# Optimization experiments

Hardware: AMD Instinct MI355X
Metric: run time of the kernel (lower is better)

The kernel has to match this reference:

```python
import jax, jax.numpy as jnp
import numpy as np

B, C, H, W = 2, 128, 64, 64
NUM_HEADS = 8
GN_GROUPS = 8
GN_EPS = 1e-5


def setup_inputs() -> dict:
    key = jax.random.key(0)
    ks = jax.random.split(key, 11)
    s = 0.02
    return {
        "x": jax.random.normal(ks[0], (B, C, H, W), dtype=jnp.float32),
        "Wq": jax.random.normal(ks[1], (C, C), dtype=jnp.float32) * s,
        "bq": jnp.zeros((C,), dtype=jnp.float32),
        "Wk": jax.random.normal(ks[2], (C, C), dtype=jnp.float32) * s,
        "bk": jnp.zeros((C,), dtype=jnp.float32),
        "Wv": jax.random.normal(ks[3], (C, C), dtype=jnp.float32) * s,
        "bv": jnp.zeros((C,), dtype=jnp.float32),
        "Wo": jax.random.normal(ks[4], (C, C), dtype=jnp.float32) * s,
        "bo": jnp.zeros((C,), dtype=jnp.float32),
        "gn_w": jnp.ones((C,), dtype=jnp.float32),
        "gn_b": jnp.zeros((C,), dtype=jnp.float32),
    }


def reference(x, Wq, bq, Wk, bk, Wv, bv, Wo, bo, gn_w, gn_b):
    b, c, h, w = x.shape
    nh = NUM_HEADS
    dh = c // nh
    scale = dh ** (-0.5)

    # [b, c, h, w] -> [b, N, c]
    x_seq = x.reshape(b, c, h * w).transpose(0, 2, 1)

    def proj(W, bias):
        y = jnp.einsum('bnc,dc->bnd', x_seq, W) + bias  # nn.Linear: x @ W.T + b
        return y.reshape(b, -1, nh, dh).transpose(0, 2, 1, 3)  # [b, nh, N, dh]

    q = proj(Wq, bq)
    k = proj(Wk, bk)
    v = proj(Wv, bv)

    attn = jnp.einsum('bhnd,bhmd->bhnm', q, k) * scale  # [b, nh, N, N]
    attn = jax.nn.softmax(attn, axis=-1)
    out = jnp.einsum('bhnm,bhmd->bhnd', attn, v)        # [b, nh, N, dh]

    out = out.transpose(0, 2, 1, 3).reshape(b, -1, c)   # [b, N, c]
    out = jnp.einsum('bnc,dc->bnd', out, Wo) + bo
    out = out.transpose(0, 2, 1).reshape(b, c, h, w)

    # GroupNorm(8, c) with affine params, then residual
    g = GN_GROUPS
    og = out.reshape(b, g, c // g, h, w)
    mean = jnp.mean(og, axis=(2, 3, 4), keepdims=True)
    var = jnp.var(og, axis=(2, 3, 4), keepdims=True)
    og = (og - mean) * jax.lax.rsqrt(var + GN_EPS)
    normed = og.reshape(b, c, h, w) * gn_w[None, :, None, None] + gn_b[None, :, None, None]
    return normed + x
```

## Files before the change

kernel.cpp:

```cpp
#include <hip/hip_runtime.h>

#define TID ((int)threadIdx.x)

constexpr int Bb  = 2;
constexpr int Cc  = 128;
constexpr int Nn  = 4096;
constexpr int NHh = 8;
constexpr int DHd = 16;
constexpr int NSP = 4;
constexpr float GN_EPS_F = 1e-5f;
constexpr float QSCALE = 0.25f * 1.4426950408889634f;

typedef float  f32x4  __attribute__((ext_vector_type(4)));
typedef float  f32x16 __attribute__((ext_vector_type(16)));
typedef short  s16x8  __attribute__((ext_vector_type(8)));
typedef unsigned short u16x8 __attribute__((ext_vector_type(8)));

#if __has_builtin(__builtin_amdgcn_exp2f)
#define EXP2(x) __builtin_amdgcn_exp2f(x)
#else
#define EXP2(x) exp2f(x)
#endif

constexpr size_t WS_PART = 0;
constexpr size_t WS_LP   = 8192;
constexpr size_t WS_AOP  = WS_LP + (size_t)NSP*16*Nn;
constexpr size_t WS_QBF  = WS_AOP + ((size_t)NSP*Bb*Nn*Cc)/2;
constexpr size_t BF_ELEMS = (size_t)Bb*NHh*Nn*DHd;

__device__ __forceinline__ ushort f2bf(float f) {
    uint u = __builtin_bit_cast(uint, f);
    u += 0x7fffu + ((u >> 16) & 1u);
    return (ushort)(u >> 16);
}
__device__ __forceinline__ float bf2f(ushort u) {
    return __builtin_bit_cast(float, ((uint)u) << 16);
}
__device__ __forceinline__ uint cvt_pk_bf16(float lo, float hi) {
    uint d;
    asm("v_cvt_pk_bf16_f32 %0, %1, %2" : "=v"(d) : "v"(lo), "v"(hi));
    return d;
}

__global__ __launch_bounds__(512) void qkv_kernel(
    const float* __restrict__ x,
    const float* __restrict__ Wq, const float* __restrict__ bq,
    const float* __restrict__ Wk, const float* __restrict__ bk,
    const float* __restrict__ Wv, const float* __restrict__ bv,
    ushort* __restrict__ qbf, ushort* __restrict__ kbf, ushort* __restrict__ vtbf)
{
    const int b  = blockIdx.x >> 7;
    const int n0 = (blockIdx.x & 127) << 5;
    __shared__ float sbuf[4356];
    const float* xb = x + (size_t)b * Cc * Nn;
    for (int i = TID; i < 32 * 128; i += 512) {
        int c = i >> 5, nl = i & 31;
        sbuf[nl * 132 + c] = xb[(size_t)c * Nn + n0 + nl];
    }
    __syncthreads();
    const int d = TID & 127, q4 = TID >> 7;
    float aq[8], ak[8], av[8];
#pragma unroll
    for (int j = 0; j < 8; ++j) { aq[j] = 0.f; ak[j] = 0.f; av[j] = 0.f; }
    const float4* wqp = (const float4*)(Wq + (size_t)d * 128);
    const float4* wkp = (const float4*)(Wk + (size_t)d * 128);
    const float4* wvp = (const float4*)(Wv + (size_t)d * 128);
#pragma unroll 4
    for (int c4 = 0; c4 < 32; ++c4) {
        float4 wq4 = wqp[c4], wk4 = wkp[c4], wv4 = wvp[c4];
#pragma unroll
        for (int j = 0; j < 8; ++j) {
            float4 xv = *(const float4*)&sbuf[(q4*8 + j) * 132 + c4 * 4];
            aq[j] += xv.x*wq4.x + xv.y*wq4.y + xv.z*wq4.z + xv.w*wq4.w;
            ak[j] += xv.x*wk4.x + xv.y*wk4.y + xv.z*wk4.z + xv.w*wk4.w;
            av[j] += xv.x*wv4.x + xv.y*wv4.y + xv.z*wv4.z + xv.w*wv4.w;
        }
    }
    const float bq_ = bq[d], bk_ = bk[d], bv_ = bv[d];

    __syncthreads();
#pragma unroll
    for (int j = 0; j < 8; ++j) sbuf[d * 33 + q4*8 + j] = (aq[j] + bq_) * QSCALE;
    __syncthreads();
    {
        int n = TID & 31, oct = TID >> 5;
        int h = oct >> 1, half8 = oct & 1;
        u16x8 u;
#pragma unroll
        for (int e = 0; e < 8; ++e) u[e] = f2bf(sbuf[(oct*8 + e) * 33 + n]);
        *(u16x8*)(qbf + ((size_t)((b*NHh + h)*Nn + n0 + n)) * DHd + half8*8) = u;
    }
    __syncthreads();
#pragma unroll
    for (int j = 0; j < 8; ++j) sbuf[d * 33 + q4*8 + j] = ak[j] + bk_;
    __syncthreads();
    {
        int n = TID & 31, oct = TID >> 5;
        int h = oct >> 1, half8 = oct & 1;
        u16x8 u;
#pragma unroll
        for (int e = 0; e < 8; ++e) u[e] = f2bf(sbuf[(oct*8 + e) * 33 + n]);
        *(u16x8*)(kbf + ((size_t)((b*NHh + h)*Nn + n0 + n)) * DHd + half8*8) = u;
    }
    __syncthreads();
#pragma unroll
    for (int j = 0; j < 8; ++j) sbuf[d * 33 + q4*8 + j] = av[j] + bv_;
    __syncthreads();
    {
        int dch = TID >> 2, qq = TID & 3;
        u16x8 u;
#pragma unroll
        for (int e = 0; e < 8; ++e) u[e] = f2bf(sbuf[dch * 33 + qq*8 + e]);
        int h = dch >> 4, dd = dch & 15;
        *(u16x8*)(vtbf + ((size_t)(b*NHh + h)*DHd + dd) * Nn + n0 + qq*8) = u;
    }
}

__global__ __launch_bounds__(256, 5) void attn_kernel(
    const ushort* __restrict__ qbf, const ushort* __restrict__ kbf,
    const ushort* __restrict__ vtbf, ushort* __restrict__ aop, float* __restrict__ lp)
{
    const int qt = blockIdx.x & 31;
    const int sp = (blockIdx.x >> 5) & 3;
    const int bh = blockIdx.x >> 7;
    const int q0 = qt << 7;
    const int kvbase = sp << 10;
    const ushort* qb  = qbf  + (size_t)bh * Nn * DHd;
    const ushort* kb  = kbf  + (size_t)bh * Nn * DHd;
    const ushort* vtb = vtbf + (size_t)bh * DHd * Nn;

    __shared__ __align__(16) ushort k_lds[64][16];
    __shared__ __align__(16) ushort vt_lds[16][88];
    __shared__ __align__(16) ushort ps[4][32][88];

    const int wave = TID >> 6, lane = TID & 63;
    const int l31 = lane & 31, hi = lane >> 5;
    const int l15 = lane & 15, g  = lane >> 4;
    const int wq = q0 + wave * 32;

    const s16x8 qfrag = *(const s16x8*)(qb + (size_t)(wq + l31) * DHd + 8 * hi);

    float l_run = 0.0f;
    f32x4 o0 = (f32x4)(0.f), o1 = (f32x4)(0.f);
    ushort* psw = &ps[wave][0][0];

    for (int kv0 = kvbase; kv0 < kvbase + 1024; kv0 += 64) {
        if (TID < 128) {
            *(u16x8*)((char*)&k_lds[0][0] + TID * 16) =
                *(const u16x8*)(kb + (size_t)kv0 * DHd + TID * 8);
        } else {
            int t = TID - 128, r = t >> 3, c8 = (t & 7) * 8;
            *(u16x8*)&vt_lds[r][c8] = *(const u16x8*)(vtb + (size_t)r * Nn + kv0 + c8);
        }
        __syncthreads();

        s16x8 af0 = *(const s16x8*)&k_lds[l31][8 * hi];
        s16x8 af1 = *(const s16x8*)&k_lds[32 + l31][8 * hi];
        f32x16 st0 = __builtin_amdgcn_mfma_f32_32x32x16_bf16(af0, qfrag, (f32x16)(0.f), 0, 0, 0);
        f32x16 st1 = __builtin_amdgcn_mfma_f32_32x32x16_bf16(af1, qfrag, (f32x16)(0.f), 0, 0, 0);

        float rs = 0.f;
        {
            float p[16];
#pragma unroll
            for (int r = 0; r < 16; ++r) { p[r] = EXP2(st0[r]); rs += p[r]; }
            char* rowp = (char*)psw + (size_t)l31 * 176;
#pragma unroll
            for (int m4 = 0; m4 < 4; ++m4) {
                uint2 w;
                w.x = cvt_pk_bf16(p[4*m4 + 0], p[4*m4 + 1]);
                w.y = cvt_pk_bf16(p[4*m4 + 2], p[4*m4 + 3]);
                *(uint2*)(rowp + 16*m4 + 8*hi) = w;
            }
        }
        {
            float p[16];
#pragma unroll
            for (int r = 0; r < 16; ++r) { p[r] = EXP2(st1[r]); rs += p[r]; }
            char* rowp = (char*)psw + (size_t)l31 * 176;
#pragma unroll
            for (int m4 = 0; m4 < 4; ++m4) {
                uint2 w;
                w.x = cvt_pk_bf16(p[4*m4 + 0], p[4*m4 + 1]);
                w.y = cvt_pk_bf16(p[4*m4 + 2], p[4*m4 + 3]);
                *(uint2*)(rowp + 16*m4 + 8*hi + 64) = w;
            }
        }
        l_run += rs;

#pragma unroll
        for (int cc = 0; cc < 2; ++cc) {
            s16x8 vf  = *(const s16x8*)&vt_lds[l15][cc*32 + 8*g];
            s16x8 pf0 = *(const s16x8*)((char*)psw + (size_t)l15 * 176        + 16*g + 64*cc);
            s16x8 pf1 = *(const s16x8*)((char*)psw + (size_t)(16 + l15) * 176 + 16*g + 64*cc);
            o0 = __builtin_amdgcn_mfma_f32_16x16x32_bf16(pf0, vf, o0, 0, 0, 0);
            o1 = __builtin_amdgcn_mfma_f32_16x16x32_bf16(pf1, vf, o1, 0, 0, 0);
        }
        __syncthreads();
    }

    l_run += __shfl_xor(l_run, 32, 64);
    if (hi == 0)
        lp[((size_t)(sp * 16 + bh)) * Nn + wq + l31] = l_run;

    const int b = bh >> 3, hh = bh & 7;
    ushort* ap = aop + (((size_t)(sp * Bb + b)) * Nn) * Cc;
#pragma unroll
    for (int r = 0; r < 4; ++r) {
        int n0r = wq + 4*g + r, n1r = wq + 16 + 4*g + r;
        ap[(size_t)n0r * Cc + hh * DHd + l15] = f2bf(o0[r]);
        ap[(size_t)n1r * Cc + hh * DHd + l15] = f2bf(o1[r]);
    }
}

__global__ __launch_bounds__(256) void oproj_kernel(
    const ushort* __restrict__ aop, const float* __restrict__ lp,
    const float* __restrict__ Wo, const float* __restrict__ bo,
    float* __restrict__ y, float* __restrict__ partial)
{
    const int b  = blockIdx.x >> 8;
    const int n0 = (blockIdx.x & 255) << 4;
    __shared__ float xs[16][132];
    __shared__ float linv[16][8];
    __shared__ float sred[16][2];

    if (TID < 128) {
        int nl = TID >> 3, h = TID & 7;
        float l = 0.f;
#pragma unroll
        for (int sp = 0; sp < NSP; ++sp)
            l += lp[((size_t)(sp * 16 + b * 8 + h)) * Nn + n0 + nl];
        linv[nl][h] = 1.0f / l;
    }
    __syncthreads();

    for (int i = TID; i < 16 * 32; i += 256) {
        int nl = i >> 5, c4 = (i & 31) * 4;
        float4 a = make_float4(0.f, 0.f, 0.f, 0.f);
#pragma unroll
        for (int sp = 0; sp < NSP; ++sp) {
            ushort4 u = *(const ushort4*)(aop + (((size_t)(sp * Bb + b)) * Nn + n0 + nl) * Cc + c4);
            a.x += bf2f(u.x); a.y += bf2f(u.y); a.z += bf2f(u.z); a.w += bf2f(u.w);
        }
        float li = linv[nl][c4 >> 4];
        xs[nl][c4 + 0] = a.x * li; xs[nl][c4 + 1] = a.y * li;
        xs[nl][c4 + 2] = a.z * li; xs[nl][c4 + 3] = a.w * li;
    }
    __syncthreads();

    const int d = TID & 127, half = TID >> 7;
    float acc[8];
#pragma unroll
    for (int j = 0; j < 8; ++j) acc[j] = 0.f;
    const float4* wop = (const float4*)(Wo + (size_t)d * 128);
#pragma unroll 4
    for (int c4 = 0; c4 < 32; ++c4) {
        float4 w4 = wop[c4];
#pragma unroll
        for (int j = 0; j < 8; ++j) {
            float4 xv = *(const float4*)&xs[half*8 + j][c4 * 4];
            acc[j] += xv.x*w4.x + xv.y*w4.y + xv.z*w4.z + xv.w*w4.w;
        }
    }
    const float bod = bo[d];
    float s1 = 0.f, s2 = 0.f;
    float* yp = y + ((size_t)(b * Cc + d)) * Nn + n0 + half * 8;
#pragma unroll
    for (int j = 0; j < 8; ++j) {
        float yv = acc[j] + bod;
        s1 += yv; s2 += yv * yv;
        yp[j] = yv;
    }
#pragma unroll
    for (int off = 1; off < 16; off <<= 1) {
        s1 += __shfl_xor(s1, off, 64);
        s2 += __shfl_xor(s2, off, 64);
    }
    if ((TID & 15) == 0) { sred[TID >> 4][0] = s1; sred[TID >> 4][1] = s2; }
    __syncthreads();
    if (TID < 8) {
        partial[((size_t)blockIdx.x * 8 + TID) * 2 + 0] = sred[TID][0] + sred[TID + 8][0];
        partial[((size_t)blockIdx.x * 8 + TID) * 2 + 1] = sred[TID][1] + sred[TID + 8][1];
    }
}

__global__ __launch_bounds__(256) void finalize_kernel(
    const float* __restrict__ x, const float* __restrict__ gn_w, const float* __restrict__ gn_b,
    const float* __restrict__ partial, float* __restrict__ out)
{
    __shared__ float red[4][2];
    const size_t i0 = (size_t)blockIdx.x << 10;
    const int b = (int)(i0 >> 19);
    const int c = (int)((i0 >> 12) & 127);
    const int g = c >> 4;

    float2 pv = *(const float2*)&partial[(((size_t)(b << 8) + TID) * 8 + g) * 2];
    float s1 = pv.x, s2 = pv.y;
#pragma unroll
    for (int off = 1; off < 64; off <<= 1) {
        s1 += __shfl_xor(s1, off, 64);
        s2 += __shfl_xor(s2, off, 64);
    }
    if ((TID & 63) == 0) { red[TID >> 6][0] = s1; red[TID >> 6][1] = s2; }
    __syncthreads();
    s1 = red[0][0] + red[1][0] + red[2][0] + red[3][0];
    s2 = red[0][1] + red[1][1] + red[2][1] + red[3][1];

    const float inv_cnt = 1.0f / 65536.0f;
    float mean = s1 * inv_cnt;
    float var  = s2 * inv_cnt - mean * mean;
    float rstd = rsqrtf(var + GN_EPS_F);
    float a   = rstd * gn_w[c];
    float bb2 = gn_b[c] - mean * a;

    size_t i = i0 + (size_t)TID * 4;
    float4 yv = *(float4*)(out + i);
    float4 xv = *(const float4*)(x + i);
    float4 o;
    o.x = yv.x * a + bb2 + xv.x;
    o.y = yv.y * a + bb2 + xv.y;
    o.z = yv.z * a + bb2 + xv.z;
    o.w = yv.w * a + bb2 + xv.w;
    *(float4*)(out + i) = o;
}

extern "C" void kernel_launch(void* const* d_in, const int* in_sizes, int n_in,
                              void* d_out, int out_size, void* d_ws, size_t ws_size,
                              hipStream_t stream) {
    const float* x  = (const float*)d_in[0];
    const float* Wq = (const float*)d_in[1];
    const float* bq = (const float*)d_in[2];
    const float* Wk = (const float*)d_in[3];
    const float* bk = (const float*)d_in[4];
    const float* Wv = (const float*)d_in[5];
    const float* bv = (const float*)d_in[6];
    const float* Wo = (const float*)d_in[7];
    const float* bo = (const float*)d_in[8];
    const float* gw = (const float*)d_in[9];
    const float* gb = (const float*)d_in[10];
    float* out = (float*)d_out;
    float* ws  = (float*)d_ws;

    float*  partial = ws + WS_PART;
    float*  lpart   = ws + WS_LP;
    ushort* aop     = (ushort*)(ws + WS_AOP);
    ushort* qbf     = (ushort*)(ws + WS_QBF);
    ushort* kbf     = qbf + BF_ELEMS;
    ushort* vtbf    = kbf + BF_ELEMS;

    hipLaunchKernelGGL(qkv_kernel, dim3(Bb * (Nn / 32)), dim3(512), 0, stream,
                       x, Wq, bq, Wk, bk, Wv, bv, qbf, kbf, vtbf);
    hipLaunchKernelGGL(attn_kernel, dim3(16 * NSP * 32), dim3(256), 0, stream,
                       qbf, kbf, vtbf, aop, lpart);
    hipLaunchKernelGGL(oproj_kernel, dim3(Bb * (Nn / 16)), dim3(256), 0, stream,
                       aop, lpart, Wo, bo, out, partial);
    hipLaunchKernelGGL(finalize_kernel, dim3((Bb * Cc * Nn) / 1024), dim3(256), 0, stream,
                       x, gw, gb, partial, out);
}
```

Measured before the change: 159.4 us.

## Move QKV and output projections to bf16 MFMA with split hi/lo precision

Adds a prep kernel that splits the weights into bf16 high and low parts, folding the Q scale into Wq. The QKV and output projection kernels then run on 32x32x16 bf16 MFMA instead of scalar FP32 FMAs. QKV uses a three-term split on both operands to stay close to FP32 accuracy, while the output projection splits only the weights and rounds the attention output to bf16. The output projection tile grows to 32 rows, and the GroupNorm partial-sum layout and finalize kernel change to match. This adds a small extra launch and weight conversion on every call.

```diff
diff --git a/kernel.cpp b/kernel.cpp
--- a/kernel.cpp
+++ b/kernel.cpp
@@ -23,10 +23,11 @@
 #endif
 
 constexpr size_t WS_PART = 0;
-constexpr size_t WS_LP   = 8192;
+constexpr size_t WS_LP   = 4096;
 constexpr size_t WS_AOP  = WS_LP + (size_t)NSP*16*Nn;
 constexpr size_t WS_QBF  = WS_AOP + ((size_t)NSP*Bb*Nn*Cc)/2;
 constexpr size_t BF_ELEMS = (size_t)Bb*NHh*Nn*DHd;
+constexpr size_t WS_W    = WS_QBF + 3*(BF_ELEMS/2);
 
 __device__ __forceinline__ ushort f2bf(float f) {
     uint u = __builtin_bit_cast(uint, f);
@@ -42,77 +43,114 @@
     return d;
 }
 
-__global__ __launch_bounds__(512) void qkv_kernel(
+__global__ __launch_bounds__(256) void prep_w_kernel(
+    const float* __restrict__ Wq, const float* __restrict__ Wk,
+    const float* __restrict__ Wv, const float* __restrict__ Wo,
+    ushort* __restrict__ wh, ushort* __restrict__ wl)
+{
+    int id = blockIdx.x * 256 + TID;
+    int which = id >> 14, i = id & 16383;
+    const float* src = (which == 0) ? Wq : (which == 1) ? Wk : (which == 2) ? Wv : Wo;
+    float v = src[i];
+    if (which == 0) v *= QSCALE;
+    ushort h = f2bf(v);
+    ushort l = f2bf(v - bf2f(h));
+    wh[id] = h;
+    wl[id] = l;
+}
+
+__global__ __launch_bounds__(256) void qkv_kernel(
     const float* __restrict__ x,
-    const float* __restrict__ Wq, const float* __restrict__ bq,
-    const float* __restrict__ Wk, const float* __restrict__ bk,
-    const float* __restrict__ Wv, const float* __restrict__ bv,
+    const float* __restrict__ bq, const float* __restrict__ bk, const float* __restrict__ bv,
+    const ushort* __restrict__ wh, const ushort* __restrict__ wl,
     ushort* __restrict__ qbf, ushort* __restrict__ kbf, ushort* __restrict__ vtbf)
 {
     const int b  = blockIdx.x >> 7;
     const int n0 = (blockIdx.x & 127) << 5;
-    __shared__ float sbuf[4356];
+    __shared__ __align__(16) ushort xh[32][136];
+    __shared__ __align__(16) ushort xl[32][136];
+
     const float* xb = x + (size_t)b * Cc * Nn;
-    for (int i = TID; i < 32 * 128; i += 512) {
-        int c = i >> 5, nl = i & 31;
-        sbuf[nl * 132 + c] = xb[(size_t)c * Nn + n0 + nl];
+    {
+        int c = TID >> 1, nh2 = (TID & 1) * 16;
+#pragma unroll
+        for (int j = 0; j < 4; ++j) {
+            float4 v4 = *(const float4*)&xb[(size_t)c * Nn + n0 + nh2 + 4*j];
+            float f[4] = {v4.x, v4.y, v4.z, v4.w};
+#pragma unroll
+            for (int e = 0; e < 4; ++e) {
+                int n = nh2 + 4*j + e;
+                ushort h = f2bf(f[e]);
+                xh[n][c] = h;
+                xl[n][c] = f2bf(f[e] - bf2f(h));
+            }
+        }
     }
     __syncthreads();
-    const int d = TID & 127, q4 = TID >> 7;
-    float aq[8], ak[8], av[8];
-#pragma unroll
-    for (int j = 0; j < 8; ++j) { aq[j] = 0.f; ak[j] = 0.f; av[j] = 0.f; }
-    const float4* wqp = (const float4*)(Wq + (size_t)d * 128);
-    const float4* wkp = (const float4*)(Wk + (size_t)d * 128);
-    const float4* wvp = (const float4*)(Wv + (size_t)d * 128);
-#pragma unroll 4
-    for (int c4 = 0; c4 < 32; ++c4) {
-        float4 wq4 = wqp[c4], wk4 = wkp[c4], wv4 = wvp[c4];
-#pragma unroll
-        for (int j = 0; j < 8; ++j) {
-            float4 xv = *(const float4*)&sbuf[(q4*8 + j) * 132 + c4 * 4];
-            aq[j] += xv.x*wq4.x + xv.y*wq4.y + xv.z*wq4.z + xv.w*wq4.w;
-            ak[j] += xv.x*wk4.x + xv.y*wk4.y + xv.z*wk4.z + xv.w*wk4.w;
-            av[j] += xv.x*wv4.x + xv.y*wv4.y + xv.z*wv4.z + xv.w*wv4.w;
-        }
-    }
-    const float bq_ = bq[d], bk_ = bk[d], bv_ = bv[d];
-
-    __syncthreads();
-#pragma unroll
-    for (int j = 0; j < 8; ++j) sbuf[d * 33 + q4*8 + j] = (aq[j] + bq_) * QSCALE;
-    __syncthreads();
+
+    const int lane = TID & 63, wave = TID >> 6;
+    const int l31 = lane & 31, hi = lane >> 5;
+    const int d0 = wave * 32;
+
+    const ushort* wqh = wh;              const ushort* wql = wl;
+    const ushort* wkh = wh + 16384;      const ushort* wkl = wl + 16384;
+    const ushort* wvh = wh + 2 * 16384;  const ushort* wvl = wl + 2 * 16384;
+
+    f32x16 qacc = (f32x16)(0.f), kacc = (f32x16)(0.f);
+    f32x16 vacc = (f32x16)(bv[d0 + l31]);
+    const size_t wrow = (size_t)(d0 + l31) * 128;
+
+#pragma unroll 2
+    for (int ks = 0; ks < 8; ++ks) {
+        const int co = ks * 16 + 8 * hi;
+        s16x8 xhf = *(const s16x8*)&xh[l31][co];
+        s16x8 xlf = *(const s16x8*)&xl[l31][co];
+        s16x8 aqh = *(const s16x8*)(wqh + wrow + co);
+        s16x8 aql = *(const s16x8*)(wql + wrow + co);
+        s16x8 akh = *(const s16x8*)(wkh + wrow + co);
+        s16x8 akl = *(const s16x8*)(wkl + wrow + co);
+        s16x8 avh = *(const s16x8*)(wvh + wrow + co);
+        s16x8 avl = *(const s16x8*)(wvl + wrow + co);
+        qacc = __builtin_amdgcn_mfma_f32_32x32x16_bf16(aqh, xhf, qacc, 0, 0, 0);
+        qacc = __builtin_amdgcn_mfma_f32_32x32x16_bf16(aql, xhf, qacc, 0, 0, 0);
+        qacc = __builtin_amdgcn_mfma_f32_32x32x16_bf16(aqh, xlf, qacc, 0, 0, 0);
+        kacc = __builtin_amdgcn_mfma_f32_32x32x16_bf16(akh, xhf, kacc, 0, 0, 0);
+        kacc = __builtin_amdgcn_mfma_f32_32x32x16_bf16(akl, xhf, kacc, 0, 0, 0);
+        kacc = __builtin_amdgcn_mfma_f32_32x32x16_bf16(akh, xlf, kacc, 0, 0, 0);
+        vacc = __builtin_amdgcn_mfma_f32_32x32x16_bf16(xhf, avh, vacc, 0, 0, 0);
+        vacc = __builtin_amdgcn_mfma_f32_32x32x16_bf16(xhf, avl, vacc, 0, 0, 0);
+        vacc = __builtin_amdgcn_mfma_f32_32x32x16_bf16(xlf, avh, vacc, 0, 0, 0);
+    }
+
     {
-        int n = TID & 31, oct = TID >> 5;
-        int h = oct >> 1, half8 = oct & 1;
-        u16x8 u;
-#pragma unroll
-        for (int e = 0; e < 8; ++e) u[e] = f2bf(sbuf[(oct*8 + e) * 33 + n]);
-        *(u16x8*)(qbf + ((size_t)((b*NHh + h)*Nn + n0 + n)) * DHd + half8*8) = u;
-    }
-    __syncthreads();
-#pragma unroll
-    for (int j = 0; j < 8; ++j) sbuf[d * 33 + q4*8 + j] = ak[j] + bk_;
-    __syncthreads();
+        const int n = n0 + l31;
+#pragma unroll
+        for (int q = 0; q < 4; ++q) {
+            const int dbase = d0 + 8*q + 4*hi;
+            const int h = dbase >> 4, dh0 = dbase & 15;
+            float4 bq4 = *(const float4*)&bq[dbase];
+            float4 bk4 = *(const float4*)&bk[dbase];
+            uint2 wq2, wk2;
+            wq2.x = cvt_pk_bf16(qacc[4*q+0] + bq4.x * QSCALE, qacc[4*q+1] + bq4.y * QSCALE);
+            wq2.y = cvt_pk_bf16(qacc[4*q+2] + bq4.z * QSCALE, qacc[4*q+3] + bq4.w * QSCALE);
+            wk2.x = cvt_pk_bf16(kacc[4*q+0] + bk4.x, kacc[4*q+1] + bk4.y);
+            wk2.y = cvt_pk_bf16(kacc[4*q+2] + bk4.z, kacc[4*q+3] + bk4.w);
+            size_t base = ((size_t)((b*NHh + h) * Nn + n)) * DHd + dh0;
+            *(uint2*)(qbf + base) = wq2;
+            *(uint2*)(kbf + base) = wk2;
+        }
+    }
     {
-        int n = TID & 31, oct = TID >> 5;
-        int h = oct >> 1, half8 = oct & 1;
-        u16x8 u;
-#pragma unroll
-        for (int e = 0; e < 8; ++e) u[e] = f2bf(sbuf[(oct*8 + e) * 33 + n]);
-        *(u16x8*)(kbf + ((size_t)((b*NHh + h)*Nn + n0 + n)) * DHd + half8*8) = u;
-    }
-    __syncthreads();
-#pragma unroll
-    for (int j = 0; j < 8; ++j) sbuf[d * 33 + q4*8 + j] = av[j] + bv_;
-    __syncthreads();
-    {
-        int dch = TID >> 2, qq = TID & 3;
-        u16x8 u;
-#pragma unroll
-        for (int e = 0; e < 8; ++e) u[e] = f2bf(sbuf[dch * 33 + qq*8 + e]);
-        int h = dch >> 4, dd = dch & 15;
-        *(u16x8*)(vtbf + ((size_t)(b*NHh + h)*DHd + dd) * Nn + n0 + qq*8) = u;
+        const int d = d0 + l31;
+        const int h = d >> 4, dd = d & 15;
+        ushort* vrow = vtbf + ((size_t)(b*NHh + h) * DHd + dd) * Nn;
+#pragma unroll
+        for (int q = 0; q < 4; ++q) {
+            uint2 w2;
+            w2.x = cvt_pk_bf16(vacc[4*q+0], vacc[4*q+1]);
+            w2.y = cvt_pk_bf16(vacc[4*q+2], vacc[4*q+3]);
+            *(uint2*)(vrow + n0 + 8*q + 4*hi) = w2;
+        }
     }
 }
 
@@ -215,72 +253,88 @@
 
 __global__ __launch_bounds__(256) void oproj_kernel(
     const ushort* __restrict__ aop, const float* __restrict__ lp,
-    const float* __restrict__ Wo, const float* __restrict__ bo,
+    const ushort* __restrict__ wh, const ushort* __restrict__ wl,
+    const float* __restrict__ bo,
     float* __restrict__ y, float* __restrict__ partial)
 {
-    const int b  = blockIdx.x >> 8;
-    const int n0 = (blockIdx.x & 255) << 4;
-    __shared__ float xs[16][132];
-    __shared__ float linv[16][8];
-    __shared__ float sred[16][2];
-
-    if (TID < 128) {
-        int nl = TID >> 3, h = TID & 7;
+    const int b  = blockIdx.x >> 7;
+    const int nb = blockIdx.x & 127;
+    const int n0 = nb << 5;
+    __shared__ __align__(16) ushort aoc[32][136];
+    __shared__ float linv[32][8];
+
+    {
+        int n = TID >> 3, h = TID & 7;
         float l = 0.f;
 #pragma unroll
         for (int sp = 0; sp < NSP; ++sp)
-            l += lp[((size_t)(sp * 16 + b * 8 + h)) * Nn + n0 + nl];
-        linv[nl][h] = 1.0f / l;
+            l += lp[((size_t)(sp * 16 + b * 8 + h)) * Nn + n0 + n];
+        linv[n][h] = 1.0f / l;
     }
     __syncthreads();
 
-    for (int i = TID; i < 16 * 32; i += 256) {
-        int nl = i >> 5, c4 = (i & 31) * 4;
-        float4 a = make_float4(0.f, 0.f, 0.f, 0.f);
+#pragma unroll
+    for (int s = TID; s < 512; s += 256) {
+        int n = s >> 4, c8 = s & 15;
+        int c = c8 * 8;
+        float a[8];
+#pragma unroll
+        for (int e = 0; e < 8; ++e) a[e] = 0.f;
 #pragma unroll
         for (int sp = 0; sp < NSP; ++sp) {
-            ushort4 u = *(const ushort4*)(aop + (((size_t)(sp * Bb + b)) * Nn + n0 + nl) * Cc + c4);
-            a.x += bf2f(u.x); a.y += bf2f(u.y); a.z += bf2f(u.z); a.w += bf2f(u.w);
-        }
-        float li = linv[nl][c4 >> 4];
-        xs[nl][c4 + 0] = a.x * li; xs[nl][c4 + 1] = a.y * li;
-        xs[nl][c4 + 2] = a.z * li; xs[nl][c4 + 3] = a.w * li;
+            u16x8 u = *(const u16x8*)(aop + (((size_t)(sp * Bb + b)) * Nn + n0 + n) * Cc + c);
+#pragma unroll
+            for (int e = 0; e < 8; ++e) a[e] += bf2f(u[e]);
+        }
+        float li = linv[n][c >> 4];
+        uint4 w;
+        w.x = cvt_pk_bf16(a[0]*li, a[1]*li);
+        w.y = cvt_pk_bf16(a[2]*li, a[3]*li);
+        w.z = cvt_pk_bf16(a[4]*li, a[5]*li);
+        w.w = cvt_pk_bf16(a[6]*li, a[7]*li);
+        *(uint4*)&aoc[n][c] = w;
     }
     __syncthreads();
 
-    const int d = TID & 127, half = TID >> 7;
-    float acc[8];
-#pragma unroll
-    for (int j = 0; j < 8; ++j) acc[j] = 0.f;
-    const float4* wop = (const float4*)(Wo + (size_t)d * 128);
-#pragma unroll 4
-    for (int c4 = 0; c4 < 32; ++c4) {
-        float4 w4 = wop[c4];
-#pragma unroll
-        for (int j = 0; j < 8; ++j) {
-            float4 xv = *(const float4*)&xs[half*8 + j][c4 * 4];
-            acc[j] += xv.x*w4.x + xv.y*w4.y + xv.z*w4.z + xv.w*w4.w;
-        }
-    }
-    const float bod = bo[d];
+    const int lane = TID & 63, wave = TID >> 6;
+    const int l31 = lane & 31, hi = lane >> 5;
+    const int d0 = wave * 32;
+    const ushort* woh = wh + 3 * 16384;
+    const ushort* wol = wl + 3 * 16384;
+    const size_t wrow = (size_t)(d0 + l31) * 128;
+
+    f32x16 acc = (f32x16)(bo[d0 + l31]);
+#pragma unroll
+    for (int ks = 0; ks < 8; ++ks) {
+        const int co = ks * 16 + 8 * hi;
+        s16x8 aof = *(const s16x8*)&aoc[l31][co];
+        s16x8 bh8 = *(const s16x8*)(woh + wrow + co);
+        s16x8 bl8 = *(const s16x8*)(wol + wrow + co);
+        acc = __builtin_amdgcn_mfma_f32_32x32x16_bf16(aof, bh8, acc, 0, 0, 0);
+        acc = __builtin_amdgcn_mfma_f32_32x32x16_bf16(aof, bl8, acc, 0, 0, 0);
+    }
+
+    const int d = d0 + l31;
+    float* yrow = y + ((size_t)(b * Cc + d)) * Nn + n0;
     float s1 = 0.f, s2 = 0.f;
-    float* yp = y + ((size_t)(b * Cc + d)) * Nn + n0 + half * 8;
-#pragma unroll
-    for (int j = 0; j < 8; ++j) {
-        float yv = acc[j] + bod;
-        s1 += yv; s2 += yv * yv;
-        yp[j] = yv;
+#pragma unroll
+    for (int q = 0; q < 4; ++q) {
+        float4 v4 = make_float4(acc[4*q+0], acc[4*q+1], acc[4*q+2], acc[4*q+3]);
+        s1 += v4.x + v4.y + v4.z + v4.w;
+        s2 += v4.x*v4.x + v4.y*v4.y + v4.z*v4.z + v4.w*v4.w;
+        *(float4*)(yrow + 8*q + 4*hi) = v4;
     }
 #pragma unroll
     for (int off = 1; off < 16; off <<= 1) {
         s1 += __shfl_xor(s1, off, 64);
         s2 += __shfl_xor(s2, off, 64);
     }
-    if ((TID & 15) == 0) { sred[TID >> 4][0] = s1; sred[TID >> 4][1] = s2; }
-    __syncthreads();
-    if (TID < 8) {
-        partial[((size_t)blockIdx.x * 8 + TID) * 2 + 0] = sred[TID][0] + sred[TID + 8][0];
-        partial[((size_t)blockIdx.x * 8 + TID) * 2 + 1] = sred[TID][1] + sred[TID + 8][1];
+    s1 += __shfl_xor(s1, 32, 64);
+    s2 += __shfl_xor(s2, 32, 64);
+    if ((lane & 15) == 0 && hi == 0) {
+        int g = d >> 4;
+        float* p = partial + (((size_t)(b * 128 + nb)) * 8 + g) * 2;
+        p[0] = s1; p[1] = s2;
     }
 }
 
@@ -294,8 +348,11 @@
     const int c = (int)((i0 >> 12) & 127);
     const int g = c >> 4;
 
-    float2 pv = *(const float2*)&partial[(((size_t)(b << 8) + TID) * 8 + g) * 2];
-    float s1 = pv.x, s2 = pv.y;
+    float s1 = 0.f, s2 = 0.f;
+    if (TID < 128) {
+        const float* p = partial + (((size_t)(b * 128 + TID)) * 8 + g) * 2;
+        s1 = p[0]; s2 = p[1];
+    }
 #pragma unroll
     for (int off = 1; off < 64; off <<= 1) {
         s1 += __shfl_xor(s1, off, 64);
@@ -347,13 +404,17 @@
     ushort* qbf     = (ushort*)(ws + WS_QBF);
     ushort* kbf     = qbf + BF_ELEMS;
     ushort* vtbf    = kbf + BF_ELEMS;
-
-    hipLaunchKernelGGL(qkv_kernel, dim3(Bb * (Nn / 32)), dim3(512), 0, stream,
-                       x, Wq, bq, Wk, bk, Wv, bv, qbf, kbf, vtbf);
+    ushort* wh      = (ushort*)(ws + WS_W);
+    ushort* wl      = wh + 4 * 16384;
+
+    hipLaunchKernelGGL(prep_w_kernel, dim3(256), dim3(256), 0, stream,
+                       Wq, Wk, Wv, Wo, wh, wl);
+    hipLaunchKernelGGL(qkv_kernel, dim3(Bb * (Nn / 32)), dim3(256), 0, stream,
+                       x, bq, bk, bv, wh, wl, qbf, kbf, vtbf);
     hipLaunchKernelGGL(attn_kernel, dim3(16 * NSP * 32), dim3(256), 0, stream,
                        qbf, kbf, vtbf, aop, lpart);
-    hipLaunchKernelGGL(oproj_kernel, dim3(Bb * (Nn / 16)), dim3(256), 0, stream,
-                       aop, lpart, Wo, bo, out, partial);
+    hipLaunchKernelGGL(oproj_kernel, dim3(Bb * (Nn / 32)), dim3(256), 0, stream,
+                       aop, lpart, wh, wl, bo, out, partial);
     hipLaunchKernelGGL(finalize_kernel, dim3((Bb * Cc * Nn) / 1024), dim3(256), 0, stream,
                        x, gw, gb, partial, out);
 }
```

Result: faster. 138.7 us (-13.0%).
